# Optimization experiments

Measured on AMD Instinct MI355X. Metric: run time of the kernel, lower is better.

## Reference

```python
import jax, jax.numpy as jnp
import numpy as np

N_NODES = 100000
N_EDGES = 1600000
IN_CH = 512
HID_CH = 256
OUT_CH = 32
K = 10


def setup_inputs() -> dict:
    key = jax.random.key(0)
    k_x, k_e, k_w1, k_b1, k_w2, k_b2 = jax.random.split(key, 6)
    x = jax.random.normal(k_x, (N_NODES, IN_CH), dtype=jnp.float32)
    edge_index = jax.random.randint(k_e, (2, N_EDGES), 0, N_NODES, dtype=jnp.int64)
    s1 = 1.0 / np.sqrt(IN_CH)
    s2 = 1.0 / np.sqrt(HID_CH)
    W1 = jax.random.uniform(k_w1, (IN_CH, HID_CH), jnp.float32, -s1, s1)
    b1 = jax.random.uniform(k_b1, (HID_CH,), jnp.float32, -s1, s1)
    W2 = jax.random.uniform(k_w2, (HID_CH, OUT_CH), jnp.float32, -s2, s2)
    b2 = jax.random.uniform(k_b2, (OUT_CH,), jnp.float32, -s2, s2)
    gamma = jnp.ones((K + 1,), jnp.float32) / (K + 1)
    return {"x": x, "edge_index": edge_index, "W1": W1, "b1": b1,
            "W2": W2, "b2": b2, "gamma": gamma}


def reference(x, edge_index, W1, b1, W2, b2, gamma):
    # MLP (dropout is identity in eval mode)
    h = jax.nn.relu(x @ W1 + b1) @ W2 + b2  # [N, out]
    row, col = edge_index[0], edge_index[1]
    # symmetric normalization: deg over destination nodes (col)
    deg = jax.ops.segment_sum(jnp.ones((N_EDGES,), h.dtype), col,
                              num_segments=N_NODES)
    deg_inv_sqrt = jnp.where(deg > 0, jax.lax.rsqrt(jnp.maximum(deg, 1.0)), 0.0)
    norm = (deg_inv_sqrt[row] * deg_inv_sqrt[col])[:, None]  # [E, 1]
    out = gamma[0] * h
    h_k = h
    for k in range(1, K + 1):
        # one hop: gather source feats, scale, scatter-add to destinations
        h_k = jax.ops.segment_sum(norm * h_k[row], col, num_segments=N_NODES)
        out = out + gamma[k] * h_k
    return out
```

## Files before the change

kernel.cpp:

```cpp
#include <hip/hip_runtime.h>
#include <hip/hip_bf16.h>

#define NN    100000
#define NE    1600000
#define INCH  512
#define HIDCH 256
#define OUTCH 32
#define KHOPS 10
#define NEPAD (NE + 3 * NN)

typedef __attribute__((ext_vector_type(8))) short short8;
typedef __attribute__((ext_vector_type(4))) float f32x4;

#define GLOAD_LDS16(gsrc, ldst) \
  __builtin_amdgcn_global_load_lds((const __attribute__((address_space(1))) void*)(gsrc), \
                                   (__attribute__((address_space(3))) void*)(ldst), 16, 0, 0)

constexpr size_t ws_align(size_t x) { return (x + 255) & ~(size_t)255; }
constexpr size_t USZ = ws_align((size_t)(NN + 1) * 32 * 2);
constexpr size_t OFF_H1   = 0;
constexpr size_t OFF_U0   = OFF_H1   + ws_align((size_t)NN*HIDCH*2);
constexpr size_t OFF_U1   = OFF_U0   + USZ;
constexpr size_t OFF_W1TH = OFF_U1   + USZ;
constexpr size_t OFF_W1TL = OFF_W1TH + ws_align((size_t)HIDCH*INCH*2);
constexpr size_t OFF_W2TH = OFF_W1TL + ws_align((size_t)HIDCH*INCH*2);
constexpr size_t OFF_W2TL = OFF_W2TH + ws_align((size_t)OUTCH*HIDCH*2);
constexpr size_t OFF_DEG  = OFF_W2TL + ws_align((size_t)OUTCH*HIDCH*2);
constexpr size_t OFF_DIS  = OFF_DEG  + ws_align((size_t)NN*4);
constexpr size_t OFF_RP   = OFF_DIS  + ws_align((size_t)NN*4);
constexpr size_t OFF_CUR  = OFF_RP   + ws_align((size_t)(NN+1)*4);
constexpr size_t OFF_CSR  = OFF_CUR  + ws_align((size_t)NN*4);
constexpr size_t OFF_PART = OFF_CSR  + ws_align((size_t)NEPAD*4);
constexpr size_t OFF_OFFS = OFF_PART + ws_align(512);

__device__ __forceinline__ unsigned short bf16_rne(float f) {
  unsigned int u = __float_as_uint(f);
  u += 0x7fffu + ((u >> 16) & 1u);
  return (unsigned short)(u >> 16);
}
__device__ __forceinline__ float bf16_to_f32(unsigned short h) {
  return __uint_as_float(((unsigned int)h) << 16);
}
__device__ __forceinline__ float bflo(unsigned int w) {
  return __uint_as_float(w << 16);
}
__device__ __forceinline__ float bfhi(unsigned int w) {
  return __uint_as_float(w & 0xffff0000u);
}

__global__ __launch_bounds__(256) void k_count_deg(const int* __restrict__ col,
                                                   int* __restrict__ deg) {
  int e = blockIdx.x * 256 + threadIdx.x;
  if (e < NE) atomicAdd(&deg[col[e]], 1);
}

__global__ __launch_bounds__(256) void k_dis(const int* __restrict__ deg,
                                             float* __restrict__ dis,
                                             unsigned short* u0, unsigned short* u1) {
  int v = blockIdx.x * 256 + threadIdx.x;
  if (v < NN) {
    int d = deg[v];
    dis[v] = d > 0 ? rsqrtf((float)d) : 0.0f;
  }
  if (blockIdx.x == 0) {
    int t = threadIdx.x;
    if (t < 16)      ((unsigned int*)u0)[(size_t)NN * 16 + t] = 0;
    else if (t < 32) ((unsigned int*)u1)[(size_t)NN * 16 + (t - 16)] = 0;
  }
}

__global__ __launch_bounds__(256) void k_scan1(const int* __restrict__ deg,
                                               int* __restrict__ rp,
                                               int* __restrict__ part) {
  __shared__ int s[256];
  int b = blockIdx.x, t = threadIdx.x;
  int base = b * 1024 + t * 4;
  int v0 = (base + 0 < NN) ? ((deg[base + 0] + 3) & ~3) : 0;
  int v1 = (base + 1 < NN) ? ((deg[base + 1] + 3) & ~3) : 0;
  int v2 = (base + 2 < NN) ? ((deg[base + 2] + 3) & ~3) : 0;
  int v3 = (base + 3 < NN) ? ((deg[base + 3] + 3) & ~3) : 0;
  int tot = v0 + v1 + v2 + v3;
  s[t] = tot;
  __syncthreads();
  for (int d = 1; d < 256; d <<= 1) {
    int x = (t >= d) ? s[t - d] : 0;
    __syncthreads();
    s[t] += x;
    __syncthreads();
  }
  int excl = s[t] - tot;
  if (t == 255) part[b] = s[255];
  if (base + 0 < NN) rp[base + 0] = excl;
  if (base + 1 < NN) rp[base + 1] = excl + v0;
  if (base + 2 < NN) rp[base + 2] = excl + v0 + v1;
  if (base + 3 < NN) rp[base + 3] = excl + v0 + v1 + v2;
}

__global__ __launch_bounds__(128) void k_scan2(const int* __restrict__ part,
                                               int* __restrict__ offs) {
  __shared__ int s[128];
  int t = threadIdx.x;
  int v = (t < 98) ? part[t] : 0;
  s[t] = v;
  __syncthreads();
  for (int d = 1; d < 128; d <<= 1) {
    int x = (t >= d) ? s[t - d] : 0;
    __syncthreads();
    s[t] += x;
    __syncthreads();
  }
  if (t < 98) offs[t] = s[t] - v;
}

__global__ __launch_bounds__(256) void k_scan3(int* __restrict__ rp,
                                               const int* __restrict__ offs,
                                               const int* __restrict__ part,
                                               int* __restrict__ cur) {
  int b = blockIdx.x, t = threadIdx.x;
  int o = offs[b];
  int base = b * 1024 + t * 4;
#pragma unroll
  for (int j = 0; j < 4; ++j) {
    int i = base + j;
    if (i < NN) {
      int r = rp[i] + o;
      rp[i] = r;
      cur[i] = r;
    }
  }
  if (b == 0 && t == 0) rp[NN] = offs[97] + part[97];
}

__global__ __launch_bounds__(256) void k_fill(const int* __restrict__ ei,
                                              int* __restrict__ cur,
                                              int* __restrict__ csrc) {
  int e = blockIdx.x * 256 + threadIdx.x;
  if (e < NE) {
    int c = ei[NE + e];
    int p = atomicAdd(&cur[c], 1);
    csrc[p] = ei[e];
  }
}

__global__ __launch_bounds__(256) void k_pad(const int* __restrict__ cur,
                                             const int* __restrict__ rp,
                                             int* __restrict__ csrc) {
  int v = blockIdx.x * 256 + threadIdx.x;
  if (v < NN) {
    int p = cur[v], e = rp[v + 1];
    for (; p < e; ++p) csrc[p] = NN;
  }
}

__global__ __launch_bounds__(256) void k_splitT(const float* __restrict__ src,
                                                unsigned short* __restrict__ dh,
                                                unsigned short* __restrict__ dl,
                                                int K, int N) {
  int idx = blockIdx.x * 256 + threadIdx.x;
  if (idx >= K * N) return;
  int n = idx / K, k = idx - n * K;
  float v = src[(size_t)k * N + n];
  unsigned short h = bf16_rne(v);
  dh[idx] = h;
  dl[idx] = bf16_rne(v - bf16_to_f32(h));
}

__global__ __launch_bounds__(512, 2) void k_gemm1(const float* __restrict__ X,
                                                  const unsigned short* __restrict__ W1Th,
                                                  const float* __restrict__ bias1,
                                                  unsigned short* __restrict__ H1bf) {
  __shared__ __align__(16) unsigned short Ah[2][4096];
  __shared__ __align__(16) unsigned short Bh[2][8192];
  const int t = threadIdx.x;
  const int m0 = blockIdx.x * 128;
  const int w = t >> 6, lane = t & 63;
  const int wm = w >> 2, wn = w & 3;

  const int arow = t >> 2;
  const int achk = t & 3;
  int axrow = m0 + arow; if (axrow >= NN) axrow = NN - 1;
  const float* aptr = X + (size_t)axrow * INCH + achk * 8;
  int aidx = (arow >> 4) * 512 + ((arow & 15) + achk * 16) * 8;
  aidx ^= ((aidx >> 7) & 3) << 4;
  const int aroff = (lane * 8) ^ (((lane >> 4) & 3) << 4);

  const int bn0 = (w * 16) + (lane & 15);
  const int bko = (lane >> 4) * 8;
  const unsigned short* bs0 = W1Th + (size_t)bn0 * INCH + bko;
  const unsigned short* bs1 = W1Th + (size_t)(bn0 + 128) * INCH + bko;

  f32x4 acc[4][4] = {};
  float4 av0, av1;

  av0 = *(const float4*)(aptr);
  av1 = *(const float4*)(aptr + 4);
  GLOAD_LDS16(bs0, &Bh[0][w * 512]);
  GLOAD_LDS16(bs1, &Bh[0][(w + 8) * 512]);
  {
    float af[8] = {av0.x, av0.y, av0.z, av0.w, av1.x, av1.y, av1.z, av1.w};
    short8 ah;
#pragma unroll
    for (int i = 0; i < 8; ++i) {
      unsigned int u = __float_as_uint(af[i]);
      ah[i] = (short)((u + 0x7fffu + ((u >> 16) & 1u)) >> 16);
    }
    *(short8*)&Ah[0][aidx] = ah;
  }
  __syncthreads();

#pragma unroll
  for (int it = 0; it < 16; ++it) {
    const int cur = it & 1, nxt = cur ^ 1;
    const int k0 = it * 32;
    if (it < 15) {
      av0 = *(const float4*)(aptr + k0 + 32);
      av1 = *(const float4*)(aptr + k0 + 36);
      GLOAD_LDS16(bs0 + k0 + 32, &Bh[nxt][w * 512]);
      GLOAD_LDS16(bs1 + k0 + 32, &Bh[nxt][(w + 8) * 512]);
    }
    short8 afrag[4];
#pragma unroll
    for (int mf = 0; mf < 4; ++mf)
      afrag[mf] = *(const short8*)&Ah[cur][(wm * 4 + mf) * 512 + aroff];
#pragma unroll
    for (int nf = 0; nf < 4; ++nf) {
      short8 bfh = *(const short8*)&Bh[cur][(wn * 4 + nf) * 512 + lane * 8];
#pragma unroll
      for (int mf = 0; mf < 4; ++mf) {
        acc[mf][nf] = __builtin_amdgcn_mfma_f32_16x16x32_bf16(afrag[mf], bfh, acc[mf][nf], 0, 0, 0);
      }
    }
    if (it < 15) {
      float af[8] = {av0.x, av0.y, av0.z, av0.w, av1.x, av1.y, av1.z, av1.w};
      short8 ah;
#pragma unroll
      for (int i = 0; i < 8; ++i) {
        unsigned int u = __float_as_uint(af[i]);
        ah[i] = (short)((u + 0x7fffu + ((u >> 16) & 1u)) >> 16);
      }
      *(short8*)&Ah[nxt][aidx] = ah;
    }
    __syncthreads();
  }

  const int colbase = wn * 64 + (lane & 15);
  const int rowbase = m0 + wm * 64 + ((lane >> 4) << 2);
#pragma unroll
  for (int nf = 0; nf < 4; ++nf) {
    int col = colbase + nf * 16;
    float b = bias1[col];
#pragma unroll
    for (int mf = 0; mf < 4; ++mf) {
#pragma unroll
      for (int r = 0; r < 4; ++r) {
        int row = rowbase + mf * 16 + r;
        if (row < NN) {
          float h = fmaxf(acc[mf][nf][r] + b, 0.f);
          H1bf[(size_t)row * HIDCH + col] = bf16_rne(h);
        }
      }
    }
  }
}

__global__ __launch_bounds__(256) void k_gemm2(const unsigned short* __restrict__ H1bf,
                                               const unsigned short* __restrict__ W2Th,
                                               const unsigned short* __restrict__ W2Tl,
                                               const float* __restrict__ bias2,
                                               const float* __restrict__ gamma,
                                               const float* __restrict__ dis,
                                               unsigned short* __restrict__ u0,
                                               float* __restrict__ out) {
  __shared__ __align__(16) unsigned short A2[8192];
  __shared__ __align__(16) unsigned short B2h[2048], B2l[2048];
  const int t = threadIdx.x;
  const int m0 = blockIdx.x * 128;

  const int arow = t >> 1;
  int axrow = m0 + arow; if (axrow >= NN) axrow = NN - 1;
  const int akb = (t & 1) * 32;
  const unsigned short* ap = H1bf + (size_t)axrow * HIDCH + akb;
  const int abase = ((arow >> 4) * 2 + (akb >> 5)) * 512 + (arow & 15) * 8;

  const int bnr = t >> 3, bkq = (t & 7) * 8;
  const int bslot = ((bnr >> 4) * 2 + (bkq >> 5)) * 512 +
                    ((bnr & 15) + (((bkq & 31) >> 3) << 4)) * 8;
  const unsigned short* bhp = W2Th + (size_t)bnr * HIDCH + bkq;
  const unsigned short* blp = W2Tl + (size_t)bnr * HIDCH + bkq;

  const int w = t >> 6, lane = t & 63;

  f32x4 acc[2][2] = {};

  for (int k0 = 0; k0 < HIDCH; k0 += 64) {
    uint4 a0 = *(const uint4*)(ap + k0);
    uint4 a1 = *(const uint4*)(ap + k0 + 8);
    uint4 a2 = *(const uint4*)(ap + k0 + 16);
    uint4 a3 = *(const uint4*)(ap + k0 + 24);
    uint4 bh = *(const uint4*)(bhp + k0);
    uint4 bl = *(const uint4*)(blp + k0);

    __syncthreads();

    *(uint4*)&A2[abase + 0 * 128] = a0;
    *(uint4*)&A2[abase + 1 * 128] = a1;
    *(uint4*)&A2[abase + 2 * 128] = a2;
    *(uint4*)&A2[abase + 3 * 128] = a3;
    *(uint4*)&B2h[bslot] = bh;
    *(uint4*)&B2l[bslot] = bl;

    __syncthreads();

    const short8* AV  = (const short8*)A2;
    const short8* BHV = (const short8*)B2h;
    const short8* BLV = (const short8*)B2l;
#pragma unroll
    for (int k32 = 0; k32 < 2; ++k32) {
      short8 bfh[2], bfl[2];
#pragma unroll
      for (int nf = 0; nf < 2; ++nf) {
        bfh[nf] = BHV[(nf * 2 + k32) * 64 + lane];
        bfl[nf] = BLV[(nf * 2 + k32) * 64 + lane];
      }
#pragma unroll
      for (int mf = 0; mf < 2; ++mf) {
        short8 a = AV[((w * 2 + mf) * 2 + k32) * 64 + lane];
#pragma unroll
        for (int nf = 0; nf < 2; ++nf) {
          acc[mf][nf] = __builtin_amdgcn_mfma_f32_16x16x32_bf16(a, bfh[nf], acc[mf][nf], 0, 0, 0);
          acc[mf][nf] = __builtin_amdgcn_mfma_f32_16x16x32_bf16(a, bfl[nf], acc[mf][nf], 0, 0, 0);
        }
      }
    }
  }

  const float g0 = gamma[0];
  const int colb = lane & 15;
  const int rowb = m0 + w * 32 + ((lane >> 4) << 2);
  const float b2c0 = bias2[colb], b2c1 = bias2[16 + colb];
#pragma unroll
  for (int mf = 0; mf < 2; ++mf) {
#pragma unroll
    for (int r = 0; r < 4; ++r) {
      int row = rowb + mf * 16 + r;
      if (row < NN) {
        float dv = dis[row];
        float h0 = acc[mf][0][r] + b2c0;
        float h1 = acc[mf][1][r] + b2c1;
        size_t o = (size_t)row * 32 + colb;
        u0[o] = bf16_rne(dv * h0);
        u0[o + 16] = bf16_rne(dv * h1);
        out[o] = g0 * h0;
        out[o + 16] = g0 * h1;
      }
    }
  }
}

__global__ __launch_bounds__(256) void k_hop(const unsigned short* __restrict__ Uin,
                                             unsigned short* __restrict__ Uout,
                                             float* __restrict__ out,
                                             const int* __restrict__ rp,
                                             const int* __restrict__ csrc,
                                             const float* __restrict__ dis,
                                             const float* __restrict__ gamma,
                                             int k) {
  const int t = threadIdx.x;
  const int g = t >> 4;
  const int li = t & 15;
  const int v = blockIdx.x * 16 + g;
  const int s = rp[v], e = rp[v + 1];
  const unsigned int* Uin32 = (const unsigned int*)Uin;

  float ax0 = 0.f, ay0 = 0.f, ax1 = 0.f, ay1 = 0.f;
  float ax2 = 0.f, ay2 = 0.f, ax3 = 0.f, ay3 = 0.f;
  int j = s;
  for (; j + 8 <= e; j += 8) {
    int4 sa = *(const int4*)&csrc[j];
    int4 sb = *(const int4*)&csrc[j + 4];
    unsigned int w0 = Uin32[(size_t)sa.x * 16 + li];
    unsigned int w1 = Uin32[(size_t)sa.y * 16 + li];
    unsigned int w2 = Uin32[(size_t)sa.z * 16 + li];
    unsigned int w3 = Uin32[(size_t)sa.w * 16 + li];
    unsigned int w4 = Uin32[(size_t)sb.x * 16 + li];
    unsigned int w5 = Uin32[(size_t)sb.y * 16 + li];
    unsigned int w6 = Uin32[(size_t)sb.z * 16 + li];
    unsigned int w7 = Uin32[(size_t)sb.w * 16 + li];
    ax0 += bflo(w0); ay0 += bfhi(w0);
    ax1 += bflo(w1); ay1 += bfhi(w1);
    ax2 += bflo(w2); ay2 += bfhi(w2);
    ax3 += bflo(w3); ay3 += bfhi(w3);
    ax0 += bflo(w4); ay0 += bfhi(w4);
    ax1 += bflo(w5); ay1 += bfhi(w5);
    ax2 += bflo(w6); ay2 += bfhi(w6);
    ax3 += bflo(w7); ay3 += bfhi(w7);
  }
  if (j < e) {
    int4 sa = *(const int4*)&csrc[j];
    unsigned int w0 = Uin32[(size_t)sa.x * 16 + li];
    unsigned int w1 = Uin32[(size_t)sa.y * 16 + li];
    unsigned int w2 = Uin32[(size_t)sa.z * 16 + li];
    unsigned int w3 = Uin32[(size_t)sa.w * 16 + li];
    ax0 += bflo(w0); ay0 += bfhi(w0);
    ax1 += bflo(w1); ay1 += bfhi(w1);
    ax2 += bflo(w2); ay2 += bfhi(w2);
    ax3 += bflo(w3); ay3 += bfhi(w3);
  }
  const float Sx = (ax0 + ax1) + (ax2 + ax3);
  const float Sy = (ay0 + ay1) + (ay2 + ay3);
  const float dv = dis[v];
  const float gd = gamma[k] * dv;
  const float d2 = dv * dv;
  unsigned int packed = (unsigned int)bf16_rne(d2 * Sx) |
                        ((unsigned int)bf16_rne(d2 * Sy) << 16);
  ((unsigned int*)Uout)[(size_t)v * 16 + li] = packed;
  const size_t o = (size_t)v * 32 + li * 2;
  float2 po = *(const float2*)&out[o];
  po.x = fmaf(gd, Sx, po.x);
  po.y = fmaf(gd, Sy, po.y);
  *(float2*)&out[o] = po;
}

extern "C" void kernel_launch(void* const* d_in, const int* in_sizes, int n_in,
                              void* d_out, int out_size, void* d_ws, size_t ws_size,
                              hipStream_t stream) {
  const float* x     = (const float*)d_in[0];
  const int*   ei    = (const int*)d_in[1];
  const float* W1    = (const float*)d_in[2];
  const float* b1    = (const float*)d_in[3];
  const float* W2    = (const float*)d_in[4];
  const float* b2    = (const float*)d_in[5];
  const float* gamma = (const float*)d_in[6];
  float* out = (float*)d_out;

  char* ws = (char*)d_ws;
  unsigned short* h1bf = (unsigned short*)(ws + OFF_H1);
  unsigned short* U[2] = {(unsigned short*)(ws + OFF_U0),
                          (unsigned short*)(ws + OFF_U1)};
  unsigned short* w1th = (unsigned short*)(ws + OFF_W1TH);
  unsigned short* w1tl = (unsigned short*)(ws + OFF_W1TL);
  unsigned short* w2th = (unsigned short*)(ws + OFF_W2TH);
  unsigned short* w2tl = (unsigned short*)(ws + OFF_W2TL);
  int*   deg  = (int*)(ws + OFF_DEG);
  float* dis  = (float*)(ws + OFF_DIS);
  int*   rp   = (int*)(ws + OFF_RP);
  int*   cur  = (int*)(ws + OFF_CUR);
  int*   csrc = (int*)(ws + OFF_CSR);
  int*   part = (int*)(ws + OFF_PART);
  int*   offs = (int*)(ws + OFF_OFFS);

  hipMemsetAsync(deg, 0, NN * sizeof(int), stream);

  k_splitT<<<(INCH * HIDCH + 255) / 256, 256, 0, stream>>>(W1, w1th, w1tl, INCH, HIDCH);
  k_splitT<<<(HIDCH * OUTCH + 255) / 256, 256, 0, stream>>>(W2, w2th, w2tl, HIDCH, OUTCH);

  k_count_deg<<<(NE + 255) / 256, 256, 0, stream>>>(ei + NE, deg);
  k_dis<<<(NN + 255) / 256, 256, 0, stream>>>(deg, dis, U[0], U[1]);
  k_scan1<<<98, 256, 0, stream>>>(deg, rp, part);
  k_scan2<<<1, 128, 0, stream>>>(part, offs);
  k_scan3<<<98, 256, 0, stream>>>(rp, offs, part, cur);
  k_fill<<<(NE + 255) / 256, 256, 0, stream>>>(ei, cur, csrc);
  k_pad<<<(NN + 255) / 256, 256, 0, stream>>>(cur, rp, csrc);

  k_gemm1<<<(NN + 127) / 128, 512, 0, stream>>>(x, w1th, b1, h1bf);
  k_gemm2<<<(NN + 127) / 128, 256, 0, stream>>>(h1bf, w2th, w2tl, b2, gamma, dis,
                                                U[0], out);

  for (int k = 1; k <= KHOPS; ++k) {
    k_hop<<<NN / 16, 256, 0, stream>>>(U[(k - 1) & 1], U[k & 1], out,
                                       rp, csrc, dis, gamma, k);
  }
}
```

Baseline: 551.1 us.

## Pre-bucket edges by destination range before CSR fill for atomic locality

Replaces the degree-count kernel with a bucketing pass that, besides counting degrees, partitions edges into 8 destination-range buckets using per-block shared-memory histograms. The CSR fill then walks each bucket so that atomics on cur and scatter writes into csrc stay within a 12.5K-node window, which should improve L2 locality. In exchange it adds an extra 8-byte-per-edge write and read pass. It also relies on a fixed bucket capacity of 204800, which random destinations with about 200K expected edges per bucket could overflow.

```diff
diff --git a/kernel.cpp b/kernel.cpp
--- a/kernel.cpp
+++ b/kernel.cpp
@@ -8,6 +8,11 @@
 #define OUTCH 32
 #define KHOPS 10
 #define NEPAD (NE + 3 * NN)
+#define NBKT  8
+#define BDIV  12500
+#define BCAP  204800
+#define EPB_A 8192
+#define EPB_B 2048
 
 typedef __attribute__((ext_vector_type(8))) short short8;
 typedef __attribute__((ext_vector_type(4))) float f32x4;
@@ -32,6 +37,8 @@
 constexpr size_t OFF_CSR  = OFF_CUR  + ws_align((size_t)NN*4);
 constexpr size_t OFF_PART = OFF_CSR  + ws_align((size_t)NEPAD*4);
 constexpr size_t OFF_OFFS = OFF_PART + ws_align(512);
+constexpr size_t OFF_BCNT = OFF_OFFS + ws_align(512);
+constexpr size_t OFF_EPK8 = OFF_BCNT + ws_align(32);
 
 __device__ __forceinline__ unsigned short bf16_rne(float f) {
   unsigned int u = __float_as_uint(f);
@@ -48,10 +55,56 @@
   return __uint_as_float(w & 0xffff0000u);
 }
 
-__global__ __launch_bounds__(256) void k_count_deg(const int* __restrict__ col,
-                                                   int* __restrict__ deg) {
-  int e = blockIdx.x * 256 + threadIdx.x;
-  if (e < NE) atomicAdd(&deg[col[e]], 1);
+__global__ __launch_bounds__(256) void k_bucket(const int* __restrict__ ei,
+                                                int* __restrict__ deg,
+                                                int* __restrict__ bcnt,
+                                                int2* __restrict__ epk8) {
+  __shared__ int hist[NBKT], rbase[NBKT], lcur[NBKT];
+  const int t = threadIdx.x;
+  const int e0 = blockIdx.x * EPB_A;
+  if (t < NBKT) hist[t] = 0;
+  __syncthreads();
+  for (int i = t; i < EPB_A; i += 256) {
+    int e = e0 + i;
+    if (e < NE) {
+      int c = ei[NE + e];
+      atomicAdd(&deg[c], 1);
+      atomicAdd(&hist[c / BDIV], 1);
+    }
+  }
+  __syncthreads();
+  if (t < NBKT) {
+    rbase[t] = atomicAdd(&bcnt[t], hist[t]);
+    lcur[t] = 0;
+  }
+  __syncthreads();
+  for (int i = t; i < EPB_A; i += 256) {
+    int e = e0 + i;
+    if (e < NE) {
+      int r = ei[e], c = ei[NE + e];
+      int b = c / BDIV;
+      int slot = atomicAdd(&lcur[b], 1);
+      epk8[(size_t)b * BCAP + rbase[b] + slot] = make_int2(r, c);
+    }
+  }
+}
+
+__global__ __launch_bounds__(256) void k_fill2(const int2* __restrict__ epk8,
+                                               const int* __restrict__ bcnt,
+                                               int* __restrict__ cur,
+                                               int* __restrict__ csrc) {
+  const int bucket = blockIdx.x & 7;
+  const int chunk = blockIdx.x >> 3;
+  const int cnt = bcnt[bucket];
+  const int lo = chunk * EPB_B;
+  int n = cnt - lo;
+  if (n > EPB_B) n = EPB_B;
+  const int2* src = epk8 + (size_t)bucket * BCAP + lo;
+  for (int i = threadIdx.x; i < n; i += 256) {
+    int2 rc = src[i];
+    int p = atomicAdd(&cur[rc.y], 1);
+    csrc[p] = rc.x;
+  }
 }
 
 __global__ __launch_bounds__(256) void k_dis(const int* __restrict__ deg,
@@ -129,17 +182,6 @@
     }
   }
   if (b == 0 && t == 0) rp[NN] = offs[97] + part[97];
-}
-
-__global__ __launch_bounds__(256) void k_fill(const int* __restrict__ ei,
-                                              int* __restrict__ cur,
-                                              int* __restrict__ csrc) {
-  int e = blockIdx.x * 256 + threadIdx.x;
-  if (e < NE) {
-    int c = ei[NE + e];
-    int p = atomicAdd(&cur[c], 1);
-    csrc[p] = ei[e];
-  }
 }
 
 __global__ __launch_bounds__(256) void k_pad(const int* __restrict__ cur,
@@ -448,18 +490,21 @@
   int*   csrc = (int*)(ws + OFF_CSR);
   int*   part = (int*)(ws + OFF_PART);
   int*   offs = (int*)(ws + OFF_OFFS);
+  int*   bcnt = (int*)(ws + OFF_BCNT);
+  int2*  epk8 = (int2*)(ws + OFF_EPK8);
 
   hipMemsetAsync(deg, 0, NN * sizeof(int), stream);
+  hipMemsetAsync(bcnt, 0, NBKT * sizeof(int), stream);
 
   k_splitT<<<(INCH * HIDCH + 255) / 256, 256, 0, stream>>>(W1, w1th, w1tl, INCH, HIDCH);
   k_splitT<<<(HIDCH * OUTCH + 255) / 256, 256, 0, stream>>>(W2, w2th, w2tl, HIDCH, OUTCH);
 
-  k_count_deg<<<(NE + 255) / 256, 256, 0, stream>>>(ei + NE, deg);
+  k_bucket<<<(NE + EPB_A - 1) / EPB_A, 256, 0, stream>>>(ei, deg, bcnt, epk8);
   k_dis<<<(NN + 255) / 256, 256, 0, stream>>>(deg, dis, U[0], U[1]);
   k_scan1<<<98, 256, 0, stream>>>(deg, rp, part);
   k_scan2<<<1, 128, 0, stream>>>(part, offs);
   k_scan3<<<98, 256, 0, stream>>>(rp, offs, part, cur);
-  k_fill<<<(NE + 255) / 256, 256, 0, stream>>>(ei, cur, csrc);
+  k_fill2<<<(BCAP / EPB_B) * NBKT, 256, 0, stream>>>(epk8, bcnt, cur, csrc);
   k_pad<<<(NN + 255) / 256, 256, 0, stream>>>(cur, rp, csrc);
 
   k_gemm1<<<(NN + 127) / 128, 512, 0, stream>>>(x, w1th, b1, h1bf);
```

Measured after the change: 527.7 us. 4.2% less time.
